# Kernel tuning notes

Hardware: AMD Instinct MI355X
Metric: run time of the kernel (lower is better)

The kernel has to match this reference:

```python
import jax, jax.numpy as jnp
import numpy as np

EPS = 1e-6
K_STEPS = 4
USE_GATING = True


def layer_norm(x, gamma, beta):
    mu = jnp.mean(x, axis=-1, keepdims=True)
    var = jnp.mean(jnp.square(x - mu), axis=-1, keepdims=True)
    return (x - mu) * jax.lax.rsqrt(var + EPS) * gamma + beta


def setup_inputs() -> dict:
    key = jax.random.key(0)
    B, L, D, H = 4, 4096, 2048, 8192
    ks = jax.random.split(key, 16)
    s = 0.02
    return {
        "x": jax.random.normal(ks[0], (B, L, D), dtype=jnp.float32),
        "in_gamma": jnp.ones((D,), jnp.float32),
        "in_beta": jnp.zeros((D,), jnp.float32),
        "agg_w": jax.random.normal(ks[1], (D, D), jnp.float32) * s,
        "agg_b": jnp.zeros((D,), jnp.float32),
        "pn_gamma": jnp.ones((D,), jnp.float32),
        "pn_beta": jnp.zeros((D,), jnp.float32),
        "d1_w": jax.random.normal(ks[2], (D, H), jnp.float32) * s,
        "d1_b": jnp.zeros((H,), jnp.float32),
        "d2_w": jax.random.normal(ks[3], (H, D), jnp.float32) * s,
        "d2_b": jnp.zeros((D,), jnp.float32),
        "bc_w": jax.random.normal(ks[4], (D, D), jnp.float32) * s,
        "bc_b": jnp.zeros((D,), jnp.float32),
        "gate_w": jax.random.normal(ks[5], (D, D), jnp.float32) * s,
        "gate_b": jnp.zeros((D,), jnp.float32),
        "out_gamma": jnp.ones((D,), jnp.float32),
        "out_beta": jnp.zeros((D,), jnp.float32),
    }


def reference(x, in_gamma, in_beta, agg_w, agg_b, pn_gamma, pn_beta,
              d1_w, d1_b, d2_w, d2_b, bc_w, bc_b, gate_w, gate_b,
              out_gamma, out_beta):
    # Input norm over the full sequence, then extract last-position summary.
    x_norm = layer_norm(x, in_gamma, in_beta)              # [B, L, D]
    thought = x_norm[:, -1, :] @ agg_w + agg_b             # [B, D]

    # Iterative pre-norm MLP thought refinement (fixed small k -> unrolled).
    for _ in range(K_STEPS):
        t = layer_norm(thought, pn_gamma, pn_beta)
        t = jax.nn.gelu(t @ d1_w + d1_b, approximate=False)
        thought = thought + (t @ d2_w + d2_b)

    # Broadcast refined thought back to every position.
    broadcast = (thought @ bc_w + bc_b)[:, None, :]        # [B, 1, D]

    if USE_GATING:
        gate = jax.nn.sigmoid(x @ gate_w + gate_b)         # [B, L, D]
        out = x + gate * broadcast
    else:
        out = x + broadcast
    return layer_norm(out, out_gamma, out_beta)
```

## Files before the change

kernel.cpp:

```cpp
#include <hip/hip_runtime.h>
#include <stdint.h>

typedef __attribute__((ext_vector_type(8))) short short8;
typedef __attribute__((ext_vector_type(4))) float f32x4;
typedef __attribute__((ext_vector_type(4))) unsigned short us4;

__device__ inline unsigned short f2bf(float f) {
    unsigned u = __float_as_uint(f);
    u = (u + 0x7FFFu + ((u >> 16) & 1u)) >> 16;
    return (unsigned short)u;
}

__device__ inline float bf2f(unsigned short u) {
    return __uint_as_float(((unsigned)u) << 16);
}

__device__ inline float gelu_f(float v) {
    return 0.5f * v * (1.0f + erff(v * 0.70710678118654752f));
}

__device__ inline void gload_lds16(const unsigned short* g, const unsigned short* l) {
    __builtin_amdgcn_global_load_lds(
        (const __attribute__((address_space(1))) unsigned int*)(g),
        (__attribute__((address_space(3))) unsigned int*)(l),
        16, 0, 0);
}

__global__ __launch_bounds__(256) void cvt_x_kernel(const float* __restrict__ in,
                                                    unsigned short* __restrict__ out, int n4) {
    int i = blockIdx.x * 256 + threadIdx.x;
    if (i >= n4) return;
    float4 v = reinterpret_cast<const float4*>(in)[i];
    us4 o = { f2bf(v.x), f2bf(v.y), f2bf(v.z), f2bf(v.w) };
    reinterpret_cast<us4*>(out)[i] = o;
}

__global__ __launch_bounds__(256) void transpose_w_kernel(const float* __restrict__ W,
                                                          unsigned short* __restrict__ WT,
                                                          int K, int N) {
    __shared__ float tile[32][33];
    int bn = blockIdx.x * 32;
    int bk = blockIdx.y * 32;
    int tx = threadIdx.x & 31;
    int ty = threadIdx.x >> 5;
#pragma unroll
    for (int j = 0; j < 32; j += 8)
        tile[ty + j][tx] = W[(long long)(bk + ty + j) * N + bn + tx];
    __syncthreads();
#pragma unroll
    for (int j = 0; j < 32; j += 8)
        WT[(long long)(bn + ty + j) * K + bk + tx] = f2bf(tile[tx][ty + j]);
}

__device__ inline void block_reduce2(float& s, float& q) {
#pragma unroll
    for (int o = 32; o > 0; o >>= 1) {
        s += __shfl_xor(s, o, 64);
        q += __shfl_xor(q, o, 64);
    }
    __shared__ float sh[8];
    __syncthreads();
    int w = threadIdx.x >> 6;
    if ((threadIdx.x & 63) == 0) { sh[w] = s; sh[4 + w] = q; }
    __syncthreads();
    s = (sh[0] + sh[1]) + (sh[2] + sh[3]);
    q = (sh[4] + sh[5]) + (sh[6] + sh[7]);
}

__global__ __launch_bounds__(256) void ln_rows_kernel(const float* __restrict__ in, long long in_stride,
                                                      float* __restrict__ out, long long out_stride,
                                                      const float* __restrict__ gamma,
                                                      const float* __restrict__ beta) {
    const float* p = in + (long long)blockIdx.x * in_stride;
    float* q = out + (long long)blockIdx.x * out_stride;
    int t = threadIdx.x;
    float4 a = reinterpret_cast<const float4*>(p)[t];
    float4 c = reinterpret_cast<const float4*>(p)[t + 256];
    float s  = (a.x + a.y) + (a.z + a.w) + (c.x + c.y) + (c.z + c.w);
    float ss = a.x*a.x + a.y*a.y + a.z*a.z + a.w*a.w
             + c.x*c.x + c.y*c.y + c.z*c.z + c.w*c.w;
    block_reduce2(s, ss);
    const float inv = 1.0f / 2048.0f;
    float mu = s * inv;
    float var = ss * inv - mu * mu;
    float rs = rsqrtf(var + 1e-6f);
    float4 g0 = reinterpret_cast<const float4*>(gamma)[t];
    float4 g1 = reinterpret_cast<const float4*>(gamma)[t + 256];
    float4 b0 = reinterpret_cast<const float4*>(beta)[t];
    float4 b1 = reinterpret_cast<const float4*>(beta)[t + 256];
    float4 o0, o1;
    o0.x = (a.x - mu) * rs * g0.x + b0.x;
    o0.y = (a.y - mu) * rs * g0.y + b0.y;
    o0.z = (a.z - mu) * rs * g0.z + b0.z;
    o0.w = (a.w - mu) * rs * g0.w + b0.w;
    o1.x = (c.x - mu) * rs * g1.x + b1.x;
    o1.y = (c.y - mu) * rs * g1.y + b1.y;
    o1.z = (c.z - mu) * rs * g1.z + b1.z;
    o1.w = (c.w - mu) * rs * g1.w + b1.w;
    reinterpret_cast<float4*>(q)[t] = o0;
    reinterpret_cast<float4*>(q)[t + 256] = o1;
}

template<int MODE>
__global__ __launch_bounds__(256) void gemv4f_kernel(const float* __restrict__ src, long long sstride,
                                                     const float* __restrict__ gamma,
                                                     const float* __restrict__ beta,
                                                     const float* __restrict__ W,
                                                     const float* __restrict__ bias,
                                                     float* __restrict__ out,
                                                     int K, int N, int KC) {
    __shared__ float sA[4][128];
    const int tid = threadIdx.x;
    const int k0 = blockIdx.y * KC;

    float mu[4], rsd[4];
    if (MODE == 1) {
#pragma unroll
        for (int r = 0; r < 4; ++r) {
            const float* p = src + r * sstride;
            float s = 0.f, q = 0.f;
            for (int k = tid; k < K; k += 256) { float v = p[k]; s += v; q += v * v; }
            block_reduce2(s, q);
            float m = s / K;
            mu[r] = m;
            rsd[r] = rsqrtf(q / K - m * m + 1e-6f);
        }
    }
    for (int idx = tid; idx < 4 * KC; idx += 256) {
        int r = idx / KC, k = idx - r * KC;
        float v = src[r * sstride + k0 + k];
        if (MODE == 1) v = (v - mu[r]) * rsd[r] * gamma[k0 + k] + beta[k0 + k];
        if (MODE == 2) v = gelu_f(v);
        sA[r][k] = v;
    }
    __syncthreads();

    const int n4 = blockIdx.x * 256 + tid;
    const int n = n4 * 4;
    const float4* W4 = reinterpret_cast<const float4*>(W);
    float4 a0 = {0.f, 0.f, 0.f, 0.f}, a1 = a0, a2 = a0, a3 = a0;
#pragma unroll 4
    for (int k = 0; k < KC; ++k) {
        float4 w = W4[((long long)(k0 + k) * N + n) >> 2];
        float c0 = sA[0][k], c1 = sA[1][k], c2 = sA[2][k], c3 = sA[3][k];
        a0.x = fmaf(c0, w.x, a0.x); a0.y = fmaf(c0, w.y, a0.y);
        a0.z = fmaf(c0, w.z, a0.z); a0.w = fmaf(c0, w.w, a0.w);
        a1.x = fmaf(c1, w.x, a1.x); a1.y = fmaf(c1, w.y, a1.y);
        a1.z = fmaf(c1, w.z, a1.z); a1.w = fmaf(c1, w.w, a1.w);
        a2.x = fmaf(c2, w.x, a2.x); a2.y = fmaf(c2, w.y, a2.y);
        a2.z = fmaf(c2, w.z, a2.z); a2.w = fmaf(c2, w.w, a2.w);
        a3.x = fmaf(c3, w.x, a3.x); a3.y = fmaf(c3, w.y, a3.y);
        a3.z = fmaf(c3, w.z, a3.z); a3.w = fmaf(c3, w.w, a3.w);
    }
    if (blockIdx.y == 0) {
        float4 b = reinterpret_cast<const float4*>(bias)[n4];
        a0.x += b.x; a0.y += b.y; a0.z += b.z; a0.w += b.w;
        a1.x += b.x; a1.y += b.y; a1.z += b.z; a1.w += b.w;
        a2.x += b.x; a2.y += b.y; a2.z += b.z; a2.w += b.w;
        a3.x += b.x; a3.y += b.y; a3.z += b.z; a3.w += b.w;
    }
    atomicAdd(&out[n + 0], a0.x); atomicAdd(&out[n + 1], a0.y);
    atomicAdd(&out[n + 2], a0.z); atomicAdd(&out[n + 3], a0.w);
    atomicAdd(&out[N + n + 0], a1.x); atomicAdd(&out[N + n + 1], a1.y);
    atomicAdd(&out[N + n + 2], a1.z); atomicAdd(&out[N + n + 3], a1.w);
    atomicAdd(&out[2 * N + n + 0], a2.x); atomicAdd(&out[2 * N + n + 1], a2.y);
    atomicAdd(&out[2 * N + n + 2], a2.z); atomicAdd(&out[2 * N + n + 3], a2.w);
    atomicAdd(&out[3 * N + n + 0], a3.x); atomicAdd(&out[3 * N + n + 1], a3.y);
    atomicAdd(&out[3 * N + n + 2], a3.z); atomicAdd(&out[3 * N + n + 3], a3.w);
}

#define BK 64
__global__ __launch_bounds__(512, 2) void gate_gemm_kernel(const unsigned short* __restrict__ A,
                                                           const unsigned short* __restrict__ BT,
                                                           const float* __restrict__ gate_b,
                                                           const float* __restrict__ bcast,
                                                           float* __restrict__ pre,
                                                           int M, int N, int K) {
    extern __shared__ unsigned short lds[];
    const int tid = threadIdx.x;
    const int lane = tid & 63;
    const int wave = tid >> 6;
    const int wm = wave >> 2;
    const int wn = wave & 3;
    const int bm0 = blockIdx.x * 256;
    const int bn0 = blockIdx.y * 256;
    const int NT = K / BK;

    const int ch0 = wave * 64 + lane;
    const int ch1 = 512 + wave * 64 + lane;
    const int r0 = ch0 >> 3, c0s = (ch0 & 7) ^ (r0 & 7);
    const int r1 = ch1 >> 3, c1s = (ch1 & 7) ^ (r1 & 7);
    const int srcoff0 = r0 * K + c0s * 8;
    const int srcoff1 = r1 * K + c1s * 8;
    const int ldso0 = ch0 * 8;
    const int ldso1 = ch1 * 8;

    const unsigned short* Abase = A + (long long)bm0 * K;
    const unsigned short* Bbase = BT + (long long)bn0 * K;

#define STAGE_A(buf, h, t)  do { \
        const unsigned short* g = Abase + (h) * 128 * K + (t) * BK; \
        const unsigned short* d = &lds[(buf) * 16384 + (h) * 8192]; \
        gload_lds16(g + srcoff0, d + ldso0); \
        gload_lds16(g + srcoff1, d + ldso1); } while (0)
#define STAGE_B(buf, h, t)  do { \
        const unsigned short* g = Bbase + (h) * 128 * K + (t) * BK; \
        const unsigned short* d = &lds[32768 + (buf) * 16384 + (h) * 8192]; \
        gload_lds16(g + srcoff0, d + ldso0); \
        gload_lds16(g + srcoff1, d + ldso1); } while (0)

    f32x4 acc[8][4];
#pragma unroll
    for (int i = 0; i < 8; ++i)
#pragma unroll
        for (int j = 0; j < 4; ++j)
#pragma unroll
            for (int r = 0; r < 4; ++r) acc[i][j][r] = 0.f;

    const int r16 = lane & 15, kq = lane >> 4;

    STAGE_A(0, 0, 0); STAGE_A(0, 1, 0);
    STAGE_B(0, 0, 0); STAGE_B(0, 1, 0);
    asm volatile("s_waitcnt vmcnt(0)" ::: "memory");
    __builtin_amdgcn_s_barrier();

    for (int t = 0; t < NT; ++t) {
        const int p = t & 1;
        const int u = t + 1;
        const int a_base = p * 16384 + wm * 8192;
        const int b_base = 32768 + p * 16384 + (wn >> 1) * 8192;

        if (u < NT) {
            STAGE_A(1 - p, 0, u); STAGE_A(1 - p, 1, u);
            STAGE_B(1 - p, 0, u); STAGE_B(1 - p, 1, u);
        }
        __builtin_amdgcn_sched_barrier(0);

        short8 bf[4][2];
#pragma unroll
        for (int ni = 0; ni < 4; ++ni) {
            const int rl = (wn & 1) * 64 + ni * 16 + r16;
#pragma unroll
            for (int kk = 0; kk < 2; ++kk)
                bf[ni][kk] = *reinterpret_cast<const short8*>(
                    &lds[b_base + rl * 64 + (((kk << 2) | kq) ^ (rl & 7)) * 8]);
        }
#pragma unroll
        for (int mh = 0; mh < 2; ++mh) {
            short8 af[4][2];
#pragma unroll
            for (int mi = 0; mi < 4; ++mi) {
                const int rl = mh * 64 + mi * 16 + r16;
#pragma unroll
                for (int kk = 0; kk < 2; ++kk)
                    af[mi][kk] = *reinterpret_cast<const short8*>(
                        &lds[a_base + rl * 64 + (((kk << 2) | kq) ^ (rl & 7)) * 8]);
            }
            __builtin_amdgcn_s_setprio(1);
#pragma unroll
            for (int mi = 0; mi < 4; ++mi)
#pragma unroll
                for (int ni = 0; ni < 4; ++ni)
#pragma unroll
                    for (int kk = 0; kk < 2; ++kk)
                        acc[mh * 4 + mi][ni] = __builtin_amdgcn_mfma_f32_16x16x32_bf16(
                            af[mi][kk], bf[ni][kk], acc[mh * 4 + mi][ni], 0, 0, 0);
            __builtin_amdgcn_s_setprio(0);
        }
        asm volatile("s_waitcnt vmcnt(0)" ::: "memory");
        __builtin_amdgcn_s_barrier();
    }

    const int bnum = bm0 >> 12;
    const float* bc_row = bcast + (long long)bnum * N;
#pragma unroll
    for (int mi = 0; mi < 8; ++mi) {
        const int row = bm0 + wm * 128 + mi * 16 + kq * 4;
#pragma unroll
        for (int ni = 0; ni < 4; ++ni) {
            const int col = bn0 + wn * 64 + ni * 16 + r16;
            const float gb = gate_b[col];
            const float bc = bc_row[col];
#pragma unroll
            for (int r = 0; r < 4; ++r) {
                const long long off = (long long)(row + r) * N + col;
                const float v = acc[mi][ni][r] + gb;
                const float g = 1.0f / (1.0f + __expf(-v));
                pre[off] = bf2f(A[off]) + g * bc;
            }
        }
    }
}
#undef STAGE_A
#undef STAGE_B

extern "C" void kernel_launch(void* const* d_in, const int* in_sizes, int n_in,
                              void* d_out, int out_size, void* d_ws, size_t ws_size,
                              hipStream_t stream) {
    const float* x         = (const float*)d_in[0];
    const float* in_gamma  = (const float*)d_in[1];
    const float* in_beta   = (const float*)d_in[2];
    const float* agg_w     = (const float*)d_in[3];
    const float* agg_b     = (const float*)d_in[4];
    const float* pn_gamma  = (const float*)d_in[5];
    const float* pn_beta   = (const float*)d_in[6];
    const float* d1_w      = (const float*)d_in[7];
    const float* d1_b      = (const float*)d_in[8];
    const float* d2_w      = (const float*)d_in[9];
    const float* d2_b      = (const float*)d_in[10];
    const float* bc_w      = (const float*)d_in[11];
    const float* bc_b      = (const float*)d_in[12];
    const float* gate_w    = (const float*)d_in[13];
    const float* gate_b    = (const float*)d_in[14];
    const float* out_gamma = (const float*)d_in[15];
    const float* out_beta  = (const float*)d_in[16];

    const int B = 4, L = 4096, D = 2048, H = 8192;
    const int M = B * L;
    float* out = (float*)d_out;

    char* ws = (char*)d_ws;
    unsigned short* xb  = (unsigned short*)ws;
    unsigned short* gwT = (unsigned short*)(ws + 67108864);
    float* tbuf  = (float*)(ws + 75497472);
    float* bcast = tbuf + 4 * D;
    float* hbuf0 = bcast + 4 * D;

    static bool attr_done = false;
    if (!attr_done) {
        hipFuncSetAttribute((const void*)gate_gemm_kernel,
                            hipFuncAttributeMaxDynamicSharedMemorySize, 131072);
        attr_done = true;
    }

    hipMemsetAsync(tbuf, 0, (4 * D + 4 * D + 4 * 4 * H) * sizeof(float), stream);

    gemv4f_kernel<1><<<dim3(D / 1024, 64), dim3(256), 0, stream>>>(
        x + (long long)(L - 1) * D, (long long)L * D, in_gamma, in_beta,
        agg_w, agg_b, tbuf, D, D, 32);

    for (int s = 0; s < 4; ++s) {
        float* hbuf = hbuf0 + s * 4 * H;
        gemv4f_kernel<1><<<dim3(H / 1024, 64), dim3(256), 0, stream>>>(
            tbuf, (long long)D, pn_gamma, pn_beta, d1_w, d1_b, hbuf, D, H, 32);
        gemv4f_kernel<2><<<dim3(D / 1024, 128), dim3(256), 0, stream>>>(
            hbuf, (long long)H, nullptr, nullptr, d2_w, d2_b, tbuf, H, D, 64);
    }
    gemv4f_kernel<0><<<dim3(D / 1024, 64), dim3(256), 0, stream>>>(
        tbuf, (long long)D, nullptr, nullptr, bc_w, bc_b, bcast, D, D, 32);

    cvt_x_kernel<<<dim3((M * D / 4) / 256), dim3(256), 0, stream>>>(x, xb, M * D / 4);
    transpose_w_kernel<<<dim3(D / 32, D / 32), dim3(256), 0, stream>>>(gate_w, gwT, D, D);

    gate_gemm_kernel<<<dim3(M / 256, D / 256), dim3(512), 131072, stream>>>(
        xb, gwT, gate_b, bcast, out, M, D, D);

    ln_rows_kernel<<<dim3(M), dim3(256), 0, stream>>>(
        out, (long long)D, out, (long long)D, out_gamma, out_beta);
}
```

Before: 602.3 us.

## Replace atomic split-K GEMV accumulation with partial buffers and reduction kernels

The small thought-refinement GEMVs no longer atomically add split-K results into the output. Each K-slice block now writes its partial result to a dedicated buffer. Separate reduce kernels sum the partials and add the bias, and the d2 GEMV folds the d1 partial reduction, bias and GELU into its input load. This removes float atomics and the memset, at the cost of more kernel launches and extra partial-buffer traffic (the d1 partials are re-read by every d2 block). It also makes the summation order deterministic.

```diff
diff --git a/kernel.cpp b/kernel.cpp
--- a/kernel.cpp
+++ b/kernel.cpp
@@ -102,19 +102,19 @@
 }
 
 template<int MODE>
-__global__ __launch_bounds__(256) void gemv4f_kernel(const float* __restrict__ src, long long sstride,
-                                                     const float* __restrict__ gamma,
-                                                     const float* __restrict__ beta,
-                                                     const float* __restrict__ W,
-                                                     const float* __restrict__ bias,
-                                                     float* __restrict__ out,
-                                                     int K, int N, int KC) {
+__global__ __launch_bounds__(256) void gemvp_kernel(const float* __restrict__ src, long long sstride,
+                                                    const float* __restrict__ gamma,
+                                                    const float* __restrict__ beta,
+                                                    const float* __restrict__ srcbias, int nY,
+                                                    const float* __restrict__ W,
+                                                    float* __restrict__ partial,
+                                                    int K, int N, int KC) {
     __shared__ float sA[4][128];
     const int tid = threadIdx.x;
     const int k0 = blockIdx.y * KC;
 
-    float mu[4], rsd[4];
     if (MODE == 1) {
+        float mu[4], rsd[4];
 #pragma unroll
         for (int r = 0; r < 4; ++r) {
             const float* p = src + r * sstride;
@@ -125,13 +125,24 @@
             mu[r] = m;
             rsd[r] = rsqrtf(q / K - m * m + 1e-6f);
         }
-    }
-    for (int idx = tid; idx < 4 * KC; idx += 256) {
-        int r = idx / KC, k = idx - r * KC;
-        float v = src[r * sstride + k0 + k];
-        if (MODE == 1) v = (v - mu[r]) * rsd[r] * gamma[k0 + k] + beta[k0 + k];
-        if (MODE == 2) v = gelu_f(v);
-        sA[r][k] = v;
+        for (int idx = tid; idx < 4 * KC; idx += 256) {
+            int r = idx / KC, k = idx - r * KC;
+            float v = src[r * sstride + k0 + k];
+            sA[r][k] = (v - mu[r]) * rsd[r] * gamma[k0 + k] + beta[k0 + k];
+        }
+    } else if (MODE == 3) {
+        for (int idx = tid; idx < 4 * KC; idx += 256) {
+            int r = idx / KC, k = idx - r * KC;
+            float acc = srcbias[k0 + k];
+            for (int y = 0; y < nY; ++y)
+                acc += src[((long long)y * 4 + r) * sstride + k0 + k];
+            sA[r][k] = gelu_f(acc);
+        }
+    } else {
+        for (int idx = tid; idx < 4 * KC; idx += 256) {
+            int r = idx / KC, k = idx - r * KC;
+            sA[r][k] = src[r * sstride + k0 + k];
+        }
     }
     __syncthreads();
 
@@ -152,21 +163,33 @@
         a3.x = fmaf(c3, w.x, a3.x); a3.y = fmaf(c3, w.y, a3.y);
         a3.z = fmaf(c3, w.z, a3.z); a3.w = fmaf(c3, w.w, a3.w);
     }
-    if (blockIdx.y == 0) {
-        float4 b = reinterpret_cast<const float4*>(bias)[n4];
-        a0.x += b.x; a0.y += b.y; a0.z += b.z; a0.w += b.w;
-        a1.x += b.x; a1.y += b.y; a1.z += b.z; a1.w += b.w;
-        a2.x += b.x; a2.y += b.y; a2.z += b.z; a2.w += b.w;
-        a3.x += b.x; a3.y += b.y; a3.z += b.z; a3.w += b.w;
-    }
-    atomicAdd(&out[n + 0], a0.x); atomicAdd(&out[n + 1], a0.y);
-    atomicAdd(&out[n + 2], a0.z); atomicAdd(&out[n + 3], a0.w);
-    atomicAdd(&out[N + n + 0], a1.x); atomicAdd(&out[N + n + 1], a1.y);
-    atomicAdd(&out[N + n + 2], a1.z); atomicAdd(&out[N + n + 3], a1.w);
-    atomicAdd(&out[2 * N + n + 0], a2.x); atomicAdd(&out[2 * N + n + 1], a2.y);
-    atomicAdd(&out[2 * N + n + 2], a2.z); atomicAdd(&out[2 * N + n + 3], a2.w);
-    atomicAdd(&out[3 * N + n + 0], a3.x); atomicAdd(&out[3 * N + n + 1], a3.y);
-    atomicAdd(&out[3 * N + n + 2], a3.z); atomicAdd(&out[3 * N + n + 3], a3.w);
+    float4* P4 = reinterpret_cast<float4*>(partial);
+    const long long pb = (long long)blockIdx.y * 4 * N;
+    P4[(pb + 0 * N + n) >> 2] = a0;
+    P4[(pb + 1 * N + n) >> 2] = a1;
+    P4[(pb + 2 * N + n) >> 2] = a2;
+    P4[(pb + 3 * N + n) >> 2] = a3;
+}
+
+template<int ACCUM>
+__global__ __launch_bounds__(256) void reduce4_kernel(const float* __restrict__ partial, int nY,
+                                                      const float* __restrict__ bias,
+                                                      float* __restrict__ out, int N) {
+    const int f4 = blockIdx.x * 256 + threadIdx.x;
+    if (f4 >= N) return;
+    const float4* P4 = reinterpret_cast<const float4*>(partial);
+    float4 acc = {0.f, 0.f, 0.f, 0.f};
+    for (int y = 0; y < nY; ++y) {
+        float4 p = P4[(long long)y * N + f4];
+        acc.x += p.x; acc.y += p.y; acc.z += p.z; acc.w += p.w;
+    }
+    float4 b = reinterpret_cast<const float4*>(bias)[f4 & (N / 4 - 1)];
+    acc.x += b.x; acc.y += b.y; acc.z += b.z; acc.w += b.w;
+    if (ACCUM) {
+        float4 o = reinterpret_cast<const float4*>(out)[f4];
+        acc.x += o.x; acc.y += o.y; acc.z += o.z; acc.w += o.w;
+    }
+    reinterpret_cast<float4*>(out)[f4] = acc;
 }
 
 #define BK 64
@@ -324,7 +347,8 @@
     unsigned short* gwT = (unsigned short*)(ws + 67108864);
     float* tbuf  = (float*)(ws + 75497472);
     float* bcast = tbuf + 4 * D;
-    float* hbuf0 = bcast + 4 * D;
+    float* P1    = bcast + 4 * D;
+    float* P2    = P1 + 64 * 4 * H;
 
     static bool attr_done = false;
     if (!attr_done) {
@@ -333,21 +357,21 @@
         attr_done = true;
     }
 
-    hipMemsetAsync(tbuf, 0, (4 * D + 4 * D + 4 * 4 * H) * sizeof(float), stream);
-
-    gemv4f_kernel<1><<<dim3(D / 1024, 64), dim3(256), 0, stream>>>(
+    gemvp_kernel<1><<<dim3(D / 1024, 64), dim3(256), 0, stream>>>(
         x + (long long)(L - 1) * D, (long long)L * D, in_gamma, in_beta,
-        agg_w, agg_b, tbuf, D, D, 32);
+        nullptr, 0, agg_w, P2, D, D, 32);
+    reduce4_kernel<0><<<dim3(D / 256), dim3(256), 0, stream>>>(P2, 64, agg_b, tbuf, D);
 
     for (int s = 0; s < 4; ++s) {
-        float* hbuf = hbuf0 + s * 4 * H;
-        gemv4f_kernel<1><<<dim3(H / 1024, 64), dim3(256), 0, stream>>>(
-            tbuf, (long long)D, pn_gamma, pn_beta, d1_w, d1_b, hbuf, D, H, 32);
-        gemv4f_kernel<2><<<dim3(D / 1024, 128), dim3(256), 0, stream>>>(
-            hbuf, (long long)H, nullptr, nullptr, d2_w, d2_b, tbuf, H, D, 64);
-    }
-    gemv4f_kernel<0><<<dim3(D / 1024, 64), dim3(256), 0, stream>>>(
-        tbuf, (long long)D, nullptr, nullptr, bc_w, bc_b, bcast, D, D, 32);
+        gemvp_kernel<1><<<dim3(H / 1024, 64), dim3(256), 0, stream>>>(
+            tbuf, (long long)D, pn_gamma, pn_beta, nullptr, 0, d1_w, P1, D, H, 32);
+        gemvp_kernel<3><<<dim3(D / 1024, 128), dim3(256), 0, stream>>>(
+            P1, (long long)H, nullptr, nullptr, d1_b, 64, d2_w, P2, H, D, 64);
+        reduce4_kernel<1><<<dim3(D / 256), dim3(256), 0, stream>>>(P2, 128, d2_b, tbuf, D);
+    }
+    gemvp_kernel<0><<<dim3(D / 1024, 64), dim3(256), 0, stream>>>(
+        tbuf, (long long)D, nullptr, nullptr, nullptr, 0, bc_w, P2, D, D, 32);
+    reduce4_kernel<0><<<dim3(D / 256), dim3(256), 0, stream>>>(P2, 64, bc_b, bcast, D);
 
     cvt_x_kernel<<<dim3((M * D / 4) / 256), dim3(256), 0, stream>>>(x, xb, M * D / 4);
     transpose_w_kernel<<<dim3(D / 32, D / 32), dim3(256), 0, stream>>>(gate_w, gwT, D, D);
```

Result: slower. 620.2 us (+3.0%).

## Fuse thought-refinement GEMV chain into one persistent kernel with grid barriers

Applied to the files above, without the earlier changes.

Replaces the sequence of separate GEMV launches (and the memset for atomics) with a single persistent 256-block kernel that runs layernorm, agg, four MLP refinement steps and the broadcast projection, separated by software grid barriers. Partial sums are written to a scratch buffer and reduced deterministically instead of using float atomics. This removes launch gaps, redundant per-block layernorm statistics, and atomic traffic, at the cost of spin-barrier synchronization and a reliance on all blocks being co-resident, with limited occupancy for streaming the weights.

```diff
diff --git a/kernel.cpp b/kernel.cpp
--- a/kernel.cpp
+++ b/kernel.cpp
@@ -4,6 +4,10 @@
 typedef __attribute__((ext_vector_type(8))) short short8;
 typedef __attribute__((ext_vector_type(4))) float f32x4;
 typedef __attribute__((ext_vector_type(4))) unsigned short us4;
+
+#define FMA4(acc, c, w) do { acc.x = fmaf((c), (w).x, acc.x); acc.y = fmaf((c), (w).y, acc.y); \
+                             acc.z = fmaf((c), (w).z, acc.z); acc.w = fmaf((c), (w).w, acc.w); } while (0)
+#define ADD4(acc, p)    do { acc.x += (p).x; acc.y += (p).y; acc.z += (p).z; acc.w += (p).w; } while (0)
 
 __device__ inline unsigned short f2bf(float f) {
     unsigned u = __float_as_uint(f);
@@ -67,13 +71,11 @@
     q = (sh[4] + sh[5]) + (sh[6] + sh[7]);
 }
 
-__global__ __launch_bounds__(256) void ln_rows_kernel(const float* __restrict__ in, long long in_stride,
-                                                      float* __restrict__ out, long long out_stride,
-                                                      const float* __restrict__ gamma,
-                                                      const float* __restrict__ beta) {
-    const float* p = in + (long long)blockIdx.x * in_stride;
-    float* q = out + (long long)blockIdx.x * out_stride;
-    int t = threadIdx.x;
+__device__ inline void ln_row_dev(const float* __restrict__ p,
+                                  const float* __restrict__ gamma,
+                                  const float* __restrict__ beta,
+                                  float* __restrict__ outp) {
+    const int t = threadIdx.x;
     float4 a = reinterpret_cast<const float4*>(p)[t];
     float4 c = reinterpret_cast<const float4*>(p)[t + 256];
     float s  = (a.x + a.y) + (a.z + a.w) + (c.x + c.y) + (c.z + c.w);
@@ -97,76 +99,175 @@
     o1.y = (c.y - mu) * rs * g1.y + b1.y;
     o1.z = (c.z - mu) * rs * g1.z + b1.z;
     o1.w = (c.w - mu) * rs * g1.w + b1.w;
-    reinterpret_cast<float4*>(q)[t] = o0;
-    reinterpret_cast<float4*>(q)[t + 256] = o1;
-}
-
-template<int MODE>
-__global__ __launch_bounds__(256) void gemv4f_kernel(const float* __restrict__ src, long long sstride,
-                                                     const float* __restrict__ gamma,
-                                                     const float* __restrict__ beta,
-                                                     const float* __restrict__ W,
-                                                     const float* __restrict__ bias,
-                                                     float* __restrict__ out,
-                                                     int K, int N, int KC) {
+    reinterpret_cast<float4*>(outp)[t] = o0;
+    reinterpret_cast<float4*>(outp)[t + 256] = o1;
+}
+
+__global__ __launch_bounds__(256) void ln_rows_kernel(const float* __restrict__ in, long long in_stride,
+                                                      float* __restrict__ out, long long out_stride,
+                                                      const float* __restrict__ gamma,
+                                                      const float* __restrict__ beta) {
+    ln_row_dev(in + (long long)blockIdx.x * in_stride, gamma, beta,
+               out + (long long)blockIdx.x * out_stride);
+}
+
+__device__ inline void gridbar(int* cnt, int target) {
+    __syncthreads();
+    if (threadIdx.x == 0) {
+        __threadfence();
+        __hip_atomic_fetch_add(cnt, 1, __ATOMIC_RELEASE, __HIP_MEMORY_SCOPE_AGENT);
+        while (__hip_atomic_load(cnt, __ATOMIC_ACQUIRE, __HIP_MEMORY_SCOPE_AGENT) < target)
+            __builtin_amdgcn_s_sleep(2);
+    }
+    __syncthreads();
+    __threadfence();
+}
+
+__device__ inline void reduce_tD(const float4* __restrict__ Pf4, const float* __restrict__ bias,
+                                 const float* __restrict__ accum, float* __restrict__ outp) {
+    const int idx = blockIdx.x * 256 + threadIdx.x;
+    const int r = idx >> 9, c4 = idx & 511;
+    float4 acc = reinterpret_cast<const float4*>(bias)[c4];
+#pragma unroll 8
+    for (int y = 0; y < 128; ++y) { float4 p = Pf4[(y * 4 + r) * 512 + c4]; ADD4(acc, p); }
+    if (accum) { float4 o = reinterpret_cast<const float4*>(accum)[idx]; ADD4(acc, o); }
+    reinterpret_cast<float4*>(outp)[idx] = acc;
+}
+
+__global__ __launch_bounds__(256, 1) void chain_kernel(
+    const float* __restrict__ x,
+    const float* __restrict__ in_gamma, const float* __restrict__ in_beta,
+    const float* __restrict__ agg_w, const float* __restrict__ agg_b,
+    const float* __restrict__ pn_gamma, const float* __restrict__ pn_beta,
+    const float* __restrict__ d1_w, const float* __restrict__ d1_b,
+    const float* __restrict__ d2_w, const float* __restrict__ d2_b,
+    const float* __restrict__ bc_w, const float* __restrict__ bc_b,
+    float* __restrict__ tln, float* __restrict__ tbuf,
+    float* __restrict__ h, float* __restrict__ bcast,
+    float* __restrict__ P, int* cnt)
+{
+    const int bid = blockIdx.x, tid = threadIdx.x;
+    int ph = 0;
     __shared__ float sA[4][128];
-    const int tid = threadIdx.x;
-    const int k0 = blockIdx.y * KC;
-
-    float mu[4], rsd[4];
-    if (MODE == 1) {
-#pragma unroll
-        for (int r = 0; r < 4; ++r) {
-            const float* p = src + r * sstride;
-            float s = 0.f, q = 0.f;
-            for (int k = tid; k < K; k += 256) { float v = p[k]; s += v; q += v * v; }
-            block_reduce2(s, q);
-            float m = s / K;
-            mu[r] = m;
-            rsd[r] = rsqrtf(q / K - m * m + 1e-6f);
-        }
-    }
-    for (int idx = tid; idx < 4 * KC; idx += 256) {
-        int r = idx / KC, k = idx - r * KC;
-        float v = src[r * sstride + k0 + k];
-        if (MODE == 1) v = (v - mu[r]) * rsd[r] * gamma[k0 + k] + beta[k0 + k];
-        if (MODE == 2) v = gelu_f(v);
-        sA[r][k] = v;
-    }
-    __syncthreads();
-
-    const int n4 = blockIdx.x * 256 + tid;
-    const int n = n4 * 4;
-    const float4* W4 = reinterpret_cast<const float4*>(W);
-    float4 a0 = {0.f, 0.f, 0.f, 0.f}, a1 = a0, a2 = a0, a3 = a0;
-#pragma unroll 4
-    for (int k = 0; k < KC; ++k) {
-        float4 w = W4[((long long)(k0 + k) * N + n) >> 2];
-        float c0 = sA[0][k], c1 = sA[1][k], c2 = sA[2][k], c3 = sA[3][k];
-        a0.x = fmaf(c0, w.x, a0.x); a0.y = fmaf(c0, w.y, a0.y);
-        a0.z = fmaf(c0, w.z, a0.z); a0.w = fmaf(c0, w.w, a0.w);
-        a1.x = fmaf(c1, w.x, a1.x); a1.y = fmaf(c1, w.y, a1.y);
-        a1.z = fmaf(c1, w.z, a1.z); a1.w = fmaf(c1, w.w, a1.w);
-        a2.x = fmaf(c2, w.x, a2.x); a2.y = fmaf(c2, w.y, a2.y);
-        a2.z = fmaf(c2, w.z, a2.z); a2.w = fmaf(c2, w.w, a2.w);
-        a3.x = fmaf(c3, w.x, a3.x); a3.y = fmaf(c3, w.y, a3.y);
-        a3.z = fmaf(c3, w.z, a3.z); a3.w = fmaf(c3, w.w, a3.w);
-    }
-    if (blockIdx.y == 0) {
-        float4 b = reinterpret_cast<const float4*>(bias)[n4];
-        a0.x += b.x; a0.y += b.y; a0.z += b.z; a0.w += b.w;
-        a1.x += b.x; a1.y += b.y; a1.z += b.z; a1.w += b.w;
-        a2.x += b.x; a2.y += b.y; a2.z += b.z; a2.w += b.w;
-        a3.x += b.x; a3.y += b.y; a3.z += b.z; a3.w += b.w;
-    }
-    atomicAdd(&out[n + 0], a0.x); atomicAdd(&out[n + 1], a0.y);
-    atomicAdd(&out[n + 2], a0.z); atomicAdd(&out[n + 3], a0.w);
-    atomicAdd(&out[N + n + 0], a1.x); atomicAdd(&out[N + n + 1], a1.y);
-    atomicAdd(&out[N + n + 2], a1.z); atomicAdd(&out[N + n + 3], a1.w);
-    atomicAdd(&out[2 * N + n + 0], a2.x); atomicAdd(&out[2 * N + n + 1], a2.y);
-    atomicAdd(&out[2 * N + n + 2], a2.z); atomicAdd(&out[2 * N + n + 3], a2.w);
-    atomicAdd(&out[3 * N + n + 0], a3.x); atomicAdd(&out[3 * N + n + 1], a3.y);
-    atomicAdd(&out[3 * N + n + 2], a3.z); atomicAdd(&out[3 * N + n + 3], a3.w);
+    float4* Pf4 = reinterpret_cast<float4*>(P);
+
+    if (bid < 4)
+        ln_row_dev(x + ((long long)bid * 4096 + 4095) * 2048, in_gamma, in_beta, tln + bid * 2048);
+    gridbar(cnt, ++ph * 256);
+
+    {
+        const int y = bid >> 1, nb = bid & 1, k0 = y * 16;
+        if (tid < 64) sA[tid >> 4][tid & 15] = tln[(tid >> 4) * 2048 + k0 + (tid & 15)];
+        __syncthreads();
+        const float4* W4 = reinterpret_cast<const float4*>(agg_w);
+        const int n4 = nb * 256 + tid;
+        float4 a0 = {0.f,0.f,0.f,0.f}, a1 = a0, a2 = a0, a3 = a0;
+#pragma unroll
+        for (int k = 0; k < 16; ++k) {
+            float4 w = W4[(k0 + k) * 512 + n4];
+            FMA4(a0, sA[0][k], w); FMA4(a1, sA[1][k], w);
+            FMA4(a2, sA[2][k], w); FMA4(a3, sA[3][k], w);
+        }
+        Pf4[(y * 4 + 0) * 512 + n4] = a0;
+        Pf4[(y * 4 + 1) * 512 + n4] = a1;
+        Pf4[(y * 4 + 2) * 512 + n4] = a2;
+        Pf4[(y * 4 + 3) * 512 + n4] = a3;
+    }
+    gridbar(cnt, ++ph * 256);
+
+    if (bid < 8) reduce_tD(Pf4, agg_b, nullptr, tbuf);
+    gridbar(cnt, ++ph * 256);
+
+    if (bid < 4) ln_row_dev(tbuf + bid * 2048, pn_gamma, pn_beta, tln + bid * 2048);
+    gridbar(cnt, ++ph * 256);
+
+    for (int s = 0; s < 4; ++s) {
+        {
+            const int kb = bid >> 3, nb = bid & 7;
+            { int r = tid >> 6, kk = tid & 63; sA[r][kk] = tln[r * 2048 + kb * 64 + kk]; }
+            __syncthreads();
+            const float4* W4 = reinterpret_cast<const float4*>(d1_w);
+            const int n4 = nb * 256 + tid;
+            float4 a0 = {0.f,0.f,0.f,0.f}, a1 = a0, a2 = a0, a3 = a0;
+#pragma unroll 8
+            for (int k = 0; k < 64; ++k) {
+                float4 w = W4[(long long)(kb * 64 + k) * 2048 + n4];
+                FMA4(a0, sA[0][k], w); FMA4(a1, sA[1][k], w);
+                FMA4(a2, sA[2][k], w); FMA4(a3, sA[3][k], w);
+            }
+            Pf4[(kb * 4 + 0) * 2048 + n4] = a0;
+            Pf4[(kb * 4 + 1) * 2048 + n4] = a1;
+            Pf4[(kb * 4 + 2) * 2048 + n4] = a2;
+            Pf4[(kb * 4 + 3) * 2048 + n4] = a3;
+        }
+        gridbar(cnt, ++ph * 256);
+
+        if (bid < 32) {
+            const int idx = bid * 256 + tid;
+            const int r = idx >> 11, c4 = idx & 2047;
+            float4 acc = reinterpret_cast<const float4*>(d1_b)[c4];
+#pragma unroll 8
+            for (int y = 0; y < 32; ++y) { float4 p = Pf4[(y * 4 + r) * 2048 + c4]; ADD4(acc, p); }
+            acc.x = gelu_f(acc.x); acc.y = gelu_f(acc.y);
+            acc.z = gelu_f(acc.z); acc.w = gelu_f(acc.w);
+            reinterpret_cast<float4*>(h)[idx] = acc;
+        }
+        gridbar(cnt, ++ph * 256);
+
+        {
+            const int kb = bid >> 2, nb = bid & 3;
+            const int kh = tid >> 7, tl = tid & 127;
+            for (int i = tid; i < 512; i += 256)
+                sA[i >> 7][i & 127] = h[(i >> 7) * 8192 + kb * 128 + (i & 127)];
+            __syncthreads();
+            const float4* W4 = reinterpret_cast<const float4*>(d2_w);
+            const int n4 = nb * 128 + tl;
+            const int k0 = kh * 64;
+            float4 a0 = {0.f,0.f,0.f,0.f}, a1 = a0, a2 = a0, a3 = a0;
+#pragma unroll 8
+            for (int k = 0; k < 64; ++k) {
+                float4 w = W4[(long long)(kb * 128 + k0 + k) * 512 + n4];
+                FMA4(a0, sA[0][k0 + k], w); FMA4(a1, sA[1][k0 + k], w);
+                FMA4(a2, sA[2][k0 + k], w); FMA4(a3, sA[3][k0 + k], w);
+            }
+            const int y = kb * 2 + kh;
+            Pf4[(y * 4 + 0) * 512 + n4] = a0;
+            Pf4[(y * 4 + 1) * 512 + n4] = a1;
+            Pf4[(y * 4 + 2) * 512 + n4] = a2;
+            Pf4[(y * 4 + 3) * 512 + n4] = a3;
+        }
+        gridbar(cnt, ++ph * 256);
+
+        if (bid < 8) reduce_tD(Pf4, d2_b, tbuf, tbuf);
+        gridbar(cnt, ++ph * 256);
+
+        if (s < 3) {
+            if (bid < 4) ln_row_dev(tbuf + bid * 2048, pn_gamma, pn_beta, tln + bid * 2048);
+            gridbar(cnt, ++ph * 256);
+        }
+    }
+
+    {
+        const int y = bid >> 1, nb = bid & 1, k0 = y * 16;
+        if (tid < 64) sA[tid >> 4][tid & 15] = tbuf[(tid >> 4) * 2048 + k0 + (tid & 15)];
+        __syncthreads();
+        const float4* W4 = reinterpret_cast<const float4*>(bc_w);
+        const int n4 = nb * 256 + tid;
+        float4 a0 = {0.f,0.f,0.f,0.f}, a1 = a0, a2 = a0, a3 = a0;
+#pragma unroll
+        for (int k = 0; k < 16; ++k) {
+            float4 w = W4[(k0 + k) * 512 + n4];
+            FMA4(a0, sA[0][k], w); FMA4(a1, sA[1][k], w);
+            FMA4(a2, sA[2][k], w); FMA4(a3, sA[3][k], w);
+        }
+        Pf4[(y * 4 + 0) * 512 + n4] = a0;
+        Pf4[(y * 4 + 1) * 512 + n4] = a1;
+        Pf4[(y * 4 + 2) * 512 + n4] = a2;
+        Pf4[(y * 4 + 3) * 512 + n4] = a3;
+    }
+    gridbar(cnt, ++ph * 256);
+
+    if (bid < 8) reduce_tD(Pf4, bc_b, nullptr, bcast);
 }
 
 #define BK 64
@@ -322,9 +423,12 @@
     char* ws = (char*)d_ws;
     unsigned short* xb  = (unsigned short*)ws;
     unsigned short* gwT = (unsigned short*)(ws + 67108864);
-    float* tbuf  = (float*)(ws + 75497472);
-    float* bcast = tbuf + 4 * D;
-    float* hbuf0 = bcast + 4 * D;
+    float* tln   = (float*)(ws + 75497472);
+    float* tbuf  = tln + 4 * D;
+    float* h     = tbuf + 4 * D;
+    float* bcast = h + 4 * H;
+    float* P     = bcast + 4 * D;
+    int*   cnt   = (int*)(P + 128 * 4 * 512 * 4);
 
     static bool attr_done = false;
     if (!attr_done) {
@@ -333,21 +437,11 @@
         attr_done = true;
     }
 
-    hipMemsetAsync(tbuf, 0, (4 * D + 4 * D + 4 * 4 * H) * sizeof(float), stream);
-
-    gemv4f_kernel<1><<<dim3(D / 1024, 64), dim3(256), 0, stream>>>(
-        x + (long long)(L - 1) * D, (long long)L * D, in_gamma, in_beta,
-        agg_w, agg_b, tbuf, D, D, 32);
-
-    for (int s = 0; s < 4; ++s) {
-        float* hbuf = hbuf0 + s * 4 * H;
-        gemv4f_kernel<1><<<dim3(H / 1024, 64), dim3(256), 0, stream>>>(
-            tbuf, (long long)D, pn_gamma, pn_beta, d1_w, d1_b, hbuf, D, H, 32);
-        gemv4f_kernel<2><<<dim3(D / 1024, 128), dim3(256), 0, stream>>>(
-            hbuf, (long long)H, nullptr, nullptr, d2_w, d2_b, tbuf, H, D, 64);
-    }
-    gemv4f_kernel<0><<<dim3(D / 1024, 64), dim3(256), 0, stream>>>(
-        tbuf, (long long)D, nullptr, nullptr, bc_w, bc_b, bcast, D, D, 32);
+    hipMemsetAsync(cnt, 0, sizeof(int), stream);
+    chain_kernel<<<dim3(256), dim3(256), 0, stream>>>(
+        x, in_gamma, in_beta, agg_w, agg_b, pn_gamma, pn_beta,
+        d1_w, d1_b, d2_w, d2_b, bc_w, bc_b,
+        tln, tbuf, h, bcast, P, cnt);
 
     cvt_x_kernel<<<dim3((M * D / 4) / 256), dim3(256), 0, stream>>>(x, xb, M * D / 4);
     transpose_w_kernel<<<dim3(D / 32, D / 32), dim3(256), 0, stream>>>(gate_w, gwT, D, D);
```

Result: slower. 1.546 ms (+156.7%).
